# Performance work log

Measured on AMD Instinct MI355X. Metric: run time of the kernel, lower is better.

The kernel has to match this reference:

```python
import jax, jax.numpy as jnp
import numpy as np

N = 100000      # nodes
E = 1600000     # edges
NW = 512        # num_words (input feature dim)
H = 128         # hidden_size
L = 3           # num_layers
G = 256         # num graphs
NEG = 0.2       # GAT leaky_relu slope
EPS = 1e-5      # batchnorm eps


def setup_inputs() -> dict:
    key = jax.random.key(0)
    ks = jax.random.split(key, 20)
    x = jax.random.normal(ks[0], (N, NW), jnp.float32)
    edge_index = jax.random.randint(ks[1], (2, E), 0, N, dtype=jnp.int64)
    edge_attr = jax.random.randint(ks[2], (E,), 0, 8, dtype=jnp.int64)
    batch = jnp.sort(jax.random.randint(ks[3], (N,), 0, G, dtype=jnp.int64))
    edge_emb = jax.random.normal(ks[4], (8, H), jnp.float32) * 0.05
    W0 = jax.random.normal(ks[5], (NW, H), jnp.float32) / np.sqrt(NW)
    W_rest = jax.random.normal(ks[6], (L - 1, H, H), jnp.float32) / np.sqrt(H)
    att_src = jax.random.normal(ks[7], (L, H), jnp.float32) / np.sqrt(H)
    att_dst = jax.random.normal(ks[8], (L, H), jnp.float32) / np.sqrt(H)
    bias = jax.random.normal(ks[9], (L, H), jnp.float32) * 0.02
    gamma = 1.0 + jax.random.normal(ks[10], (L, H), jnp.float32) * 0.1
    beta = jax.random.normal(ks[11], (L, H), jnp.float32) * 0.02
    gate_w1 = jax.random.normal(ks[12], (H, H), jnp.float32) / np.sqrt(H)
    gate_b1 = jnp.zeros((H,), jnp.float32)
    gate_w2 = jax.random.normal(ks[13], (H, 1), jnp.float32) / np.sqrt(H)
    gate_b2 = jnp.zeros((1,), jnp.float32)
    cls_w = jax.random.normal(ks[14], (H, 2), jnp.float32) / np.sqrt(H)
    cls_b = jnp.zeros((2,), jnp.float32)
    return {"x": x, "edge_index": edge_index, "edge_attr": edge_attr, "batch": batch,
            "edge_emb": edge_emb, "W0": W0, "W_rest": W_rest, "att_src": att_src,
            "att_dst": att_dst, "bias": bias, "gamma": gamma, "beta": beta,
            "gate_w1": gate_w1, "gate_b1": gate_b1, "gate_w2": gate_w2,
            "gate_b2": gate_b2, "cls_w": cls_w, "cls_b": cls_b}


def _gat_layer(x, W, a_s, a_d, b, src, dst):
    # PyG GATConv, heads=1, concat=True: h = xW; e_ij = leaky(a_s.h_src + a_d.h_dst)
    h = x @ W                                   # [N, H]
    a_src = h @ a_s                             # [N]
    a_dst = h @ a_d                             # [N]
    e = jax.nn.leaky_relu(a_src[src] + a_dst[dst], NEG)      # [E+N]
    m = jax.ops.segment_max(e, dst, num_segments=N)          # scatter-softmax over dst
    ex = jnp.exp(e - m[dst])
    den = jax.ops.segment_sum(ex, dst, num_segments=N)
    coef = ex / den[dst]                                      # [E+N]
    out = jax.ops.segment_sum(h[src] * coef[:, None], dst, num_segments=N)
    return out + b


def _batchnorm_relu(x, g, bt):
    mu = jnp.mean(x, axis=0)
    var = jnp.mean((x - mu) ** 2, axis=0)      # biased variance (torch BN forward)
    return jax.nn.relu((x - mu) * jax.lax.rsqrt(var + EPS) * g + bt)


def reference(x, edge_index, edge_attr, batch, edge_emb, W0, W_rest, att_src,
              att_dst, bias, gamma, beta, gate_w1, gate_b1, gate_w2, gate_b2,
              cls_w, cls_b):
    _ = edge_emb[edge_attr]  # computed in original module but never used (DCE'd)
    # add self-loops as GATConv does by default
    loop = jnp.arange(N, dtype=edge_index.dtype)
    src = jnp.concatenate([edge_index[0], loop])
    dst = jnp.concatenate([edge_index[1], loop])
    Ws = [W0] + [W_rest[i] for i in range(L - 1)]
    for i in range(L):
        x = _gat_layer(x, Ws[i], att_src[i], att_dst[i], bias[i], src, dst)
        x = _batchnorm_relu(x, gamma[i], beta[i])  # dropout is identity in eval
    # GlobalAttention pooling: gate = MLP(x) -> segment softmax over graphs
    gate = jax.nn.relu(x @ gate_w1 + gate_b1) @ gate_w2 + gate_b2   # [N, 1]
    gate = gate[:, 0]
    gm = jax.ops.segment_max(gate, batch, num_segments=G)
    gex = jnp.exp(gate - gm[batch])
    gden = jax.ops.segment_sum(gex, batch, num_segments=G)
    gden = jnp.where(gden == 0, 1.0, gden)
    coef = gex / gden[batch]
    pooled = jax.ops.segment_sum(x * coef[:, None], batch, num_segments=G)  # [G, H]
    logits = pooled @ cls_w + cls_b
    return jax.nn.log_softmax(logits, axis=-1)
```

## Files before the change

### kernel.cpp

```cpp
#include <hip/hip_runtime.h>

#define kN  100000
#define kE  1600000
#define kNW 512
#define kH  128
#define kL  3
#define kG  256
#define kNEG 0.2f
#define kEPS 1e-5f

static __device__ __forceinline__ float lrelu(float v) { return v >= 0.f ? v : kNEG * v; }

__global__ void count_deg(const int* __restrict__ ei, int* __restrict__ deg, int E) {
    int e = blockIdx.x * 256 + threadIdx.x;
    if (e < E) atomicAdd(&deg[ei[E + e]], 1);
}

__global__ void scan1(const int* __restrict__ deg, int* __restrict__ bsums, int n) {
    __shared__ int sdata[256];
    int b = blockIdx.x, t = threadIdx.x;
    int base = b * 1024 + t * 4;
    int s = 0;
#pragma unroll
    for (int j = 0; j < 4; j++) { int i = base + j; s += (i < n) ? deg[i] : 0; }
    sdata[t] = s; __syncthreads();
    for (int st = 128; st > 0; st >>= 1) { if (t < st) sdata[t] += sdata[t + st]; __syncthreads(); }
    if (t == 0) bsums[b] = sdata[0];
}

__global__ void scan2(int* __restrict__ bsums, int nb, int* __restrict__ row_ptr_last) {
    __shared__ int lds[128];
    int t = threadIdx.x;
    int v = (t < nb) ? bsums[t] : 0;
    lds[t] = v; __syncthreads();
    for (int st = 1; st < 128; st <<= 1) {
        int x = 0;
        if (t >= st) x = lds[t - st];
        __syncthreads();
        if (t >= st) lds[t] += x;
        __syncthreads();
    }
    if (t < nb) bsums[t] = lds[t] - v;
    if (t == nb - 1) row_ptr_last[0] = lds[t];
}

__global__ void scan3(const int* __restrict__ deg, const int* __restrict__ bsums,
                      int* __restrict__ row_ptr, int* __restrict__ cursor, int n) {
    __shared__ int lds[256];
    int b = blockIdx.x, t = threadIdx.x;
    int base = b * 1024 + t * 4;
    int v[4]; int s = 0;
#pragma unroll
    for (int j = 0; j < 4; j++) { int i = base + j; v[j] = (i < n) ? deg[i] : 0; s += v[j]; }
    lds[t] = s; __syncthreads();
    for (int st = 1; st < 256; st <<= 1) {
        int x = 0;
        if (t >= st) x = lds[t - st];
        __syncthreads();
        if (t >= st) lds[t] += x;
        __syncthreads();
    }
    int excl = (t == 0) ? 0 : lds[t - 1];
    excl += bsums[b];
    int run = excl;
#pragma unroll
    for (int j = 0; j < 4; j++) {
        int i = base + j;
        if (i < n) { row_ptr[i] = run; cursor[i] = run; run += v[j]; }
    }
}

__global__ void fill_csr(const int* __restrict__ ei, int* __restrict__ cursor,
                         int* __restrict__ col_src, int E) {
    int e = blockIdx.x * 256 + threadIdx.x;
    if (e < E) {
        int s = ei[e], d = ei[E + e];
        int p = atomicAdd(&cursor[d], 1);
        col_src[p] = s;
    }
}

__global__ __launch_bounds__(256) void gemm128(const float* __restrict__ A,
                                               const float* __restrict__ B,
                                               float* __restrict__ C, int M, int K,
                                               const float* __restrict__ bias, int do_relu) {
    __shared__ float As[32][132];
    __shared__ float Bs[32][128];
    int tid = threadIdx.x;
    int bm = blockIdx.x * 128;
    int ty = tid >> 4;
    int tx = tid & 15;
    float acc[8][8];
#pragma unroll
    for (int i = 0; i < 8; i++)
#pragma unroll
        for (int j = 0; j < 8; j++) acc[i][j] = 0.f;

    for (int k0 = 0; k0 < K; k0 += 32) {
#pragma unroll
        for (int l = 0; l < 4; l++) {
            int f = tid + l * 256;
            int r = f >> 3;
            int c4 = f & 7;
            int gr = bm + r;
            float4 v = make_float4(0.f, 0.f, 0.f, 0.f);
            if (gr < M) v = *(const float4*)(A + (size_t)gr * K + k0 + c4 * 4);
            As[c4 * 4 + 0][r] = v.x;
            As[c4 * 4 + 1][r] = v.y;
            As[c4 * 4 + 2][r] = v.z;
            As[c4 * 4 + 3][r] = v.w;
        }
#pragma unroll
        for (int l = 0; l < 4; l++) {
            int f = tid + l * 256;
            int r = f >> 5;
            int c4 = f & 31;
            *(float4*)&Bs[r][c4 * 4] = *(const float4*)(B + (size_t)(k0 + r) * 128 + c4 * 4);
        }
        __syncthreads();
#pragma unroll
        for (int kk = 0; kk < 32; kk++) {
            float4 a0 = *(float4*)&As[kk][ty * 8];
            float4 a1 = *(float4*)&As[kk][ty * 8 + 4];
            float4 b0 = *(float4*)&Bs[kk][tx * 4];
            float4 b1 = *(float4*)&Bs[kk][64 + tx * 4];
            float aa[8] = {a0.x, a0.y, a0.z, a0.w, a1.x, a1.y, a1.z, a1.w};
            float bb[8] = {b0.x, b0.y, b0.z, b0.w, b1.x, b1.y, b1.z, b1.w};
#pragma unroll
            for (int i = 0; i < 8; i++)
#pragma unroll
                for (int j = 0; j < 8; j++) acc[i][j] += aa[i] * bb[j];
        }
        __syncthreads();
    }
#pragma unroll
    for (int i = 0; i < 8; i++) {
        int gr = bm + ty * 8 + i;
        if (gr >= M) continue;
#pragma unroll
        for (int half = 0; half < 2; half++) {
            int gc = half * 64 + tx * 4;
            float4 v;
            v.x = acc[i][half * 4 + 0]; v.y = acc[i][half * 4 + 1];
            v.z = acc[i][half * 4 + 2]; v.w = acc[i][half * 4 + 3];
            if (bias) { v.x += bias[gc]; v.y += bias[gc + 1]; v.z += bias[gc + 2]; v.w += bias[gc + 3]; }
            if (do_relu) {
                v.x = fmaxf(v.x, 0.f); v.y = fmaxf(v.y, 0.f);
                v.z = fmaxf(v.z, 0.f); v.w = fmaxf(v.w, 0.f);
            }
            *(float4*)(C + (size_t)gr * 128 + gc) = v;
        }
    }
}

__global__ void att_dots(const float* __restrict__ h, const float* __restrict__ ws_,
                         const float* __restrict__ wd_, float* __restrict__ a_s,
                         float* __restrict__ a_d, int n) {
    int v = blockIdx.x * 4 + (threadIdx.x >> 6);
    int lane = threadIdx.x & 63;
    if (v >= n) return;
    float2 hx = ((const float2*)(h + (size_t)v * 128))[lane];
    float2 ws = ((const float2*)ws_)[lane];
    float2 wd = ((const float2*)wd_)[lane];
    float ps = hx.x * ws.x + hx.y * ws.y;
    float pd = hx.x * wd.x + hx.y * wd.y;
#pragma unroll
    for (int off = 32; off; off >>= 1) {
        ps += __shfl_xor(ps, off);
        pd += __shfl_xor(pd, off);
    }
    if (lane == 0) { a_s[v] = ps; a_d[v] = pd; }
}

__global__ void edge_softmax(const int* __restrict__ row_ptr, const int* __restrict__ col_src,
                             const float* __restrict__ a_s, const float* __restrict__ a_d,
                             float* __restrict__ coef, float* __restrict__ coef_self, int n) {
    int v = blockIdx.x * 4 + (threadIdx.x >> 6);
    int lane = threadIdx.x & 63;
    if (v >= n) return;
    int s0 = row_ptr[v], s1 = row_ptr[v + 1];
    float adv = a_d[v];
    float es = lrelu(a_s[v] + adv);
    float mx = es;
    for (int k = s0 + lane; k < s1; k += 64) {
        float e = lrelu(a_s[col_src[k]] + adv);
        coef[k] = e;
        mx = fmaxf(mx, e);
    }
#pragma unroll
    for (int off = 32; off; off >>= 1) mx = fmaxf(mx, __shfl_xor(mx, off));
    float sum = 0.f;
    for (int k = s0 + lane; k < s1; k += 64) {
        float ex = expf(coef[k] - mx);
        coef[k] = ex;
        sum += ex;
    }
    if (lane == 0) sum += expf(es - mx);
#pragma unroll
    for (int off = 32; off; off >>= 1) sum += __shfl_xor(sum, off);
    float inv = 1.f / sum;
    for (int k = s0 + lane; k < s1; k += 64) coef[k] *= inv;
    if (lane == 0) coef_self[v] = expf(es - mx) * inv;
}

__global__ void aggregate(const int* __restrict__ row_ptr, const int* __restrict__ col_src,
                          const float* __restrict__ coef, const float* __restrict__ coef_self,
                          const float* __restrict__ h, const float* __restrict__ bias,
                          float* __restrict__ out, int n) {
    int v = blockIdx.x * 4 + (threadIdx.x >> 6);
    int lane = threadIdx.x & 63;
    if (v >= n) return;
    int s0 = row_ptr[v], s1 = row_ptr[v + 1];
    const float2* h2 = (const float2*)h;
    float cs = coef_self[v];
    float2 hv = h2[(size_t)v * 64 + lane];
    float ax = cs * hv.x, ay = cs * hv.y;
    for (int k = s0; k < s1; k++) {
        int s = col_src[k];
        float c = coef[k];
        float2 hs = h2[(size_t)s * 64 + lane];
        ax += c * hs.x;
        ay += c * hs.y;
    }
    float2 b = ((const float2*)bias)[lane];
    float2 o; o.x = ax + b.x; o.y = ay + b.y;
    ((float2*)out)[(size_t)v * 64 + lane] = o;
}

__global__ void bn_stats(const float* __restrict__ x, double* __restrict__ sums, int n) {
    int col = threadIdx.x & 127;
    int half = threadIdx.x >> 7;
    double s = 0.0, q = 0.0;
    for (int r = blockIdx.x * 2 + half; r < n; r += gridDim.x * 2) {
        float v = x[(size_t)r * 128 + col];
        s += v;
        q += (double)v * (double)v;
    }
    __shared__ double ls[256], lq[256];
    ls[threadIdx.x] = s; lq[threadIdx.x] = q;
    __syncthreads();
    if (half == 0) {
        s += ls[threadIdx.x + 128];
        q += lq[threadIdx.x + 128];
        atomicAdd(&sums[col], s);
        atomicAdd(&sums[128 + col], q);
    }
}

__global__ void bn_finalize(const double* __restrict__ sums, const float* __restrict__ gamma,
                            const float* __restrict__ beta, float* __restrict__ coefs, int n) {
    int c = threadIdx.x;
    if (c < 128) {
        double mu = sums[c] / n;
        double var = sums[128 + c] / n - mu * mu;
        double rs = 1.0 / sqrt(var + (double)kEPS);
        float sc = (float)rs * gamma[c];
        coefs[c] = sc;
        coefs[128 + c] = beta[c] - (float)(mu * rs) * gamma[c];
    }
}

__global__ void bn_apply(float* __restrict__ x, const float* __restrict__ coefs, int n) {
    int idx = blockIdx.x * 256 + threadIdx.x;
    if (idx >= n * 32) return;
    float4 v = ((const float4*)x)[idx];
    int c = (idx & 31) * 4;
    v.x = fmaxf(v.x * coefs[c + 0] + coefs[128 + c + 0], 0.f);
    v.y = fmaxf(v.y * coefs[c + 1] + coefs[128 + c + 1], 0.f);
    v.z = fmaxf(v.z * coefs[c + 2] + coefs[128 + c + 2], 0.f);
    v.w = fmaxf(v.w * coefs[c + 3] + coefs[128 + c + 3], 0.f);
    ((float4*)x)[idx] = v;
}

__global__ void gate_dot(const float* __restrict__ hidden, const float* __restrict__ gw2,
                         const float* __restrict__ gb2, float* __restrict__ gate, int n) {
    int v = blockIdx.x * 4 + (threadIdx.x >> 6);
    int lane = threadIdx.x & 63;
    if (v >= n) return;
    float2 hx = ((const float2*)(hidden + (size_t)v * 128))[lane];
    float2 w = ((const float2*)gw2)[lane];
    float p = hx.x * w.x + hx.y * w.y;
#pragma unroll
    for (int off = 32; off; off >>= 1) p += __shfl_xor(p, off);
    if (lane == 0) gate[v] = p + gb2[0];
}

__global__ void graph_bounds(const int* __restrict__ batch, int* __restrict__ gstart, int n, int g) {
    int i = blockIdx.x * 256 + threadIdx.x;
    if (i > g) return;
    int lo = 0, hi = n;
    while (lo < hi) {
        int mid = (lo + hi) >> 1;
        if (batch[mid] < i) lo = mid + 1; else hi = mid;
    }
    gstart[i] = lo;
}

__global__ __launch_bounds__(512) void pool(const float* __restrict__ x, const float* __restrict__ gate,
                                            const int* __restrict__ gstart, float* __restrict__ pooled) {
    int g = blockIdx.x;
    int t = threadIdx.x;
    int col = t & 127;
    int q = t >> 7;
    int s0 = gstart[g], s1 = gstart[g + 1];
    __shared__ float red[8];
    __shared__ float acc_lds[512];
    float mx = -INFINITY;
    for (int v = s0 + t; v < s1; v += 512) mx = fmaxf(mx, gate[v]);
#pragma unroll
    for (int off = 32; off; off >>= 1) mx = fmaxf(mx, __shfl_xor(mx, off));
    if ((t & 63) == 0) red[t >> 6] = mx;
    __syncthreads();
    mx = fmaxf(fmaxf(fmaxf(red[0], red[1]), fmaxf(red[2], red[3])),
               fmaxf(fmaxf(red[4], red[5]), fmaxf(red[6], red[7])));
    __syncthreads();
    float sum = 0.f;
    for (int v = s0 + t; v < s1; v += 512) sum += expf(gate[v] - mx);
#pragma unroll
    for (int off = 32; off; off >>= 1) sum += __shfl_xor(sum, off);
    if ((t & 63) == 0) red[t >> 6] = sum;
    __syncthreads();
    sum = red[0] + red[1] + red[2] + red[3] + red[4] + red[5] + red[6] + red[7];
    if (sum == 0.f) sum = 1.f;
    float inv = 1.f / sum;
    float acc = 0.f;
    for (int v = s0 + q; v < s1; v += 4) {
        float c = expf(gate[v] - mx) * inv;
        acc += x[(size_t)v * 128 + col] * c;
    }
    acc_lds[t] = acc;
    __syncthreads();
    if (q == 0)
        pooled[(size_t)g * 128 + col] = acc_lds[col] + acc_lds[128 + col] +
                                        acc_lds[256 + col] + acc_lds[384 + col];
}

__global__ void classify(const float* __restrict__ pooled, const float* __restrict__ cls_w,
                         const float* __restrict__ cls_b, float* __restrict__ out, int g_) {
    int g = blockIdx.x * 4 + (threadIdx.x >> 6);
    int lane = threadIdx.x & 63;
    if (g >= g_) return;
    float2 p = ((const float2*)(pooled + (size_t)g * 128))[lane];
    float4 w = ((const float4*)cls_w)[lane];
    float l0 = p.x * w.x + p.y * w.z;
    float l1 = p.x * w.y + p.y * w.w;
#pragma unroll
    for (int off = 32; off; off >>= 1) {
        l0 += __shfl_xor(l0, off);
        l1 += __shfl_xor(l1, off);
    }
    if (lane == 0) {
        l0 += cls_b[0]; l1 += cls_b[1];
        float m = fmaxf(l0, l1);
        float lse = m + logf(expf(l0 - m) + expf(l1 - m));
        out[g * 2 + 0] = l0 - lse;
        out[g * 2 + 1] = l1 - lse;
    }
}

extern "C" void kernel_launch(void* const* d_in, const int* in_sizes, int n_in,
                              void* d_out, int out_size, void* d_ws, size_t ws_size,
                              hipStream_t stream) {
    const float* x        = (const float*)d_in[0];
    const int*   ei       = (const int*)d_in[1];
    const int*   batch    = (const int*)d_in[3];
    const float* W0       = (const float*)d_in[5];
    const float* W_rest   = (const float*)d_in[6];
    const float* att_src  = (const float*)d_in[7];
    const float* att_dst  = (const float*)d_in[8];
    const float* bias     = (const float*)d_in[9];
    const float* gamma    = (const float*)d_in[10];
    const float* beta     = (const float*)d_in[11];
    const float* gate_w1  = (const float*)d_in[12];
    const float* gate_b1  = (const float*)d_in[13];
    const float* gate_w2  = (const float*)d_in[14];
    const float* gate_b2  = (const float*)d_in[15];
    const float* cls_w    = (const float*)d_in[16];
    const float* cls_b    = (const float*)d_in[17];
    float* out = (float*)d_out;

    char* ws = (char*)d_ws;
    size_t off = 0;
    auto take = [&](size_t bytes) -> void* {
        void* p = ws + off;
        off += (bytes + 255) & ~(size_t)255;
        return p;
    };
    float* h         = (float*)take((size_t)kN * kH * 4);
    float* xa        = (float*)take((size_t)kN * kH * 4);
    float* a_s       = (float*)take((size_t)kN * 4);
    float* a_d       = (float*)take((size_t)kN * 4);
    float* coef_self = (float*)take((size_t)kN * 4);
    int*   deg       = (int*)take((size_t)kN * 4);
    int*   cursor    = (int*)take((size_t)kN * 4);
    int*   row_ptr   = (int*)take((size_t)(kN + 1) * 4);
    int*   col_src   = (int*)take((size_t)kE * 4);
    float* coef_csr  = (float*)take((size_t)kE * 4);
    int*   bsums     = (int*)take(1024 * 4);
    double* bn_sums  = (double*)take(256 * 8);
    float* bn_coefs  = (float*)take(256 * 4);
    float* gate      = (float*)take((size_t)kN * 4);
    int*   gstart    = (int*)take((size_t)(kG + 1) * 4);
    float* pooled    = (float*)take((size_t)kG * kH * 4);
    (void)ws_size; (void)in_sizes; (void)n_in; (void)out_size;

    const int NB = (kN + 1023) / 1024;

    hipMemsetAsync(deg, 0, (size_t)kN * 4, stream);
    count_deg<<<(kE + 255) / 256, 256, 0, stream>>>(ei, deg, kE);
    scan1<<<NB, 256, 0, stream>>>(deg, bsums, kN);
    scan2<<<1, 128, 0, stream>>>(bsums, NB, row_ptr + kN);
    scan3<<<NB, 256, 0, stream>>>(deg, bsums, row_ptr, cursor, kN);
    fill_csr<<<(kE + 255) / 256, 256, 0, stream>>>(ei, cursor, col_src, kE);

    const float* xin = x;
    int K = kNW;
    for (int l = 0; l < kL; l++) {
        const float* W = (l == 0) ? W0 : (W_rest + (size_t)(l - 1) * kH * kH);
        gemm128<<<(kN + 127) / 128, 256, 0, stream>>>(xin, W, h, kN, K, nullptr, 0);
        att_dots<<<(kN + 3) / 4, 256, 0, stream>>>(h, att_src + (size_t)l * kH,
                                                   att_dst + (size_t)l * kH, a_s, a_d, kN);
        edge_softmax<<<(kN + 3) / 4, 256, 0, stream>>>(row_ptr, col_src, a_s, a_d,
                                                       coef_csr, coef_self, kN);
        aggregate<<<(kN + 3) / 4, 256, 0, stream>>>(row_ptr, col_src, coef_csr, coef_self,
                                                    h, bias + (size_t)l * kH, xa, kN);
        hipMemsetAsync(bn_sums, 0, 256 * 8, stream);
        bn_stats<<<1024, 256, 0, stream>>>(xa, bn_sums, kN);
        bn_finalize<<<1, 128, 0, stream>>>(bn_sums, gamma + (size_t)l * kH,
                                           beta + (size_t)l * kH, bn_coefs, kN);
        bn_apply<<<((kN * 32) + 255) / 256, 256, 0, stream>>>(xa, bn_coefs, kN);
        xin = xa;
        K = kH;
    }

    gemm128<<<(kN + 127) / 128, 256, 0, stream>>>(xa, gate_w1, h, kN, kH, gate_b1, 1);
    gate_dot<<<(kN + 3) / 4, 256, 0, stream>>>(h, gate_w2, gate_b2, gate, kN);

    graph_bounds<<<2, 256, 0, stream>>>(batch, gstart, kN, kG);
    pool<<<kG, 512, 0, stream>>>(xa, gate, gstart, pooled);
    classify<<<(kG + 3) / 4, 256, 0, stream>>>(pooled, cls_w, cls_b, out, kG);
}
```

Measured before the change: 1.705 ms.

## Replace FP32 SIMT GEMMs with split-bf16 MFMA GEMMs using prepacked operand tiles

Swaps the FP32 shared-memory GEMM for a matrix-core kernel that emulates FP32 with a three-term bf16 hi/lo split (hi*hi + hi*lo + lo*hi). Activations and weights are prepacked into an MFMA fragment layout, and BN-apply now writes the packed bf16 pair for the next layer's GEMM directly. The first-layer K=512 GEMM is split into two K=256 passes that accumulate into the output. This is meant to cut GEMM compute time, at the cost of extra packing passes and workspace traffic and a small loss of accuracy versus true FP32.

New measurement: 1.613 ms. -5.4%, faster.

```diff
diff --git a/kernel.cpp b/kernel.cpp
--- a/kernel.cpp
+++ b/kernel.cpp
@@ -9,7 +9,18 @@
 #define kNEG 0.2f
 #define kEPS 1e-5f
 
+typedef __attribute__((ext_vector_type(8))) short bf16x8;
+typedef __attribute__((ext_vector_type(4))) float f32x4;
+
 static __device__ __forceinline__ float lrelu(float v) { return v >= 0.f ? v : kNEG * v; }
+
+static __device__ __forceinline__ unsigned short bf16rn(float x) {
+    unsigned u = __float_as_uint(x);
+    return (unsigned short)((u + 0x7FFFu + ((u >> 16) & 1u)) >> 16);
+}
+static __device__ __forceinline__ float bf16tof(unsigned short h) {
+    return __uint_as_float(((unsigned)h) << 16);
+}
 
 __global__ void count_deg(const int* __restrict__ ei, int* __restrict__ deg, int E) {
     int e = blockIdx.x * 256 + threadIdx.x;
@@ -80,75 +91,124 @@
     }
 }
 
-__global__ __launch_bounds__(256) void gemm128(const float* __restrict__ A,
-                                               const float* __restrict__ B,
-                                               float* __restrict__ C, int M, int K,
-                                               const float* __restrict__ bias, int do_relu) {
-    __shared__ float As[32][132];
-    __shared__ float Bs[32][128];
+__global__ void pack_a(const float* __restrict__ A, unsigned short* __restrict__ apk,
+                       int Kpitch, int kbase, int NKT) {
+    int g = blockIdx.x * 256 + threadIdx.x;
+    int lane = g & 63;
+    int t2 = g >> 6;
+    int kt = t2 % NKT;
+    int rt = t2 / NKT;
+    int row = rt * 16 + (lane & 15);
+    int k0 = kbase + kt * 32 + (lane >> 4) * 8;
+    const float* src = A + (size_t)row * Kpitch + k0;
+    float4 v0 = *(const float4*)src;
+    float4 v1 = *(const float4*)(src + 4);
+    float v[8] = {v0.x, v0.y, v0.z, v0.w, v1.x, v1.y, v1.z, v1.w};
+    unsigned short h[8], l[8];
+#pragma unroll
+    for (int j = 0; j < 8; j++) {
+        h[j] = bf16rn(v[j]);
+        l[j] = bf16rn(v[j] - bf16tof(h[j]));
+    }
+    size_t slot = ((size_t)(rt * NKT + kt) * 2) * 512 + lane * 8;
+    int4 vhi = make_int4((unsigned)h[0] | ((unsigned)h[1] << 16), (unsigned)h[2] | ((unsigned)h[3] << 16),
+                         (unsigned)h[4] | ((unsigned)h[5] << 16), (unsigned)h[6] | ((unsigned)h[7] << 16));
+    int4 vlo = make_int4((unsigned)l[0] | ((unsigned)l[1] << 16), (unsigned)l[2] | ((unsigned)l[3] << 16),
+                         (unsigned)l[4] | ((unsigned)l[5] << 16), (unsigned)l[6] | ((unsigned)l[7] << 16));
+    *(int4*)(apk + slot) = vhi;
+    *(int4*)(apk + slot + 512) = vlo;
+}
+
+__global__ void pack_b_all(const float* __restrict__ W0, const float* __restrict__ Wr,
+                           const float* __restrict__ Gw1,
+                           unsigned short* __restrict__ b0a, unsigned short* __restrict__ b0b,
+                           unsigned short* __restrict__ b1, unsigned short* __restrict__ b2,
+                           unsigned short* __restrict__ bg) {
+    int bid = blockIdx.x;
+    const float* src; unsigned short* dst; int kbase; int NKT; int lb;
+    if (bid < 16)      { src = W0;            dst = b0a; kbase = 0;   NKT = 8; lb = bid; }
+    else if (bid < 32) { src = W0;            dst = b0b; kbase = 256; NKT = 8; lb = bid - 16; }
+    else if (bid < 40) { src = Wr;            dst = b1;  kbase = 0;   NKT = 4; lb = bid - 32; }
+    else if (bid < 48) { src = Wr + 128*128;  dst = b2;  kbase = 0;   NKT = 4; lb = bid - 40; }
+    else               { src = Gw1;           dst = bg;  kbase = 0;   NKT = 4; lb = bid - 48; }
+    int g = lb * 256 + threadIdx.x;
+    int lane = g & 63;
+    int t2 = g >> 6;
+    int kt = t2 % NKT;
+    int ct = t2 / NKT;
+    int col = ct * 16 + (lane & 15);
+    int k0 = kbase + kt * 32 + (lane >> 4) * 8;
+    unsigned short h[8], l[8];
+#pragma unroll
+    for (int j = 0; j < 8; j++) {
+        float v = src[(size_t)(k0 + j) * 128 + col];
+        h[j] = bf16rn(v);
+        l[j] = bf16rn(v - bf16tof(h[j]));
+    }
+    size_t slot = ((size_t)(ct * NKT + kt) * 2) * 512 + lane * 8;
+    int4 vhi = make_int4((unsigned)h[0] | ((unsigned)h[1] << 16), (unsigned)h[2] | ((unsigned)h[3] << 16),
+                         (unsigned)h[4] | ((unsigned)h[5] << 16), (unsigned)h[6] | ((unsigned)h[7] << 16));
+    int4 vlo = make_int4((unsigned)l[0] | ((unsigned)l[1] << 16), (unsigned)l[2] | ((unsigned)l[3] << 16),
+                         (unsigned)l[4] | ((unsigned)l[5] << 16), (unsigned)l[6] | ((unsigned)l[7] << 16));
+    *(int4*)(dst + slot) = vhi;
+    *(int4*)(dst + slot + 512) = vlo;
+}
+
+__global__ __launch_bounds__(256) void gemm_mfma(const unsigned short* __restrict__ apk,
+                                                 const unsigned short* __restrict__ bpk,
+                                                 float* __restrict__ C, int M, int NKT,
+                                                 int accum, const float* __restrict__ bias,
+                                                 int do_relu) {
     int tid = threadIdx.x;
-    int bm = blockIdx.x * 128;
-    int ty = tid >> 4;
-    int tx = tid & 15;
-    float acc[8][8];
-#pragma unroll
-    for (int i = 0; i < 8; i++)
-#pragma unroll
-        for (int j = 0; j < 8; j++) acc[i][j] = 0.f;
-
-    for (int k0 = 0; k0 < K; k0 += 32) {
-#pragma unroll
-        for (int l = 0; l < 4; l++) {
-            int f = tid + l * 256;
-            int r = f >> 3;
-            int c4 = f & 7;
-            int gr = bm + r;
-            float4 v = make_float4(0.f, 0.f, 0.f, 0.f);
-            if (gr < M) v = *(const float4*)(A + (size_t)gr * K + k0 + c4 * 4);
-            As[c4 * 4 + 0][r] = v.x;
-            As[c4 * 4 + 1][r] = v.y;
-            As[c4 * 4 + 2][r] = v.z;
-            As[c4 * 4 + 3][r] = v.w;
+    int w = tid >> 6, lane = tid & 63;
+    int rt0 = blockIdx.x * 8 + (w >> 1) * 4;
+    int ct0 = (w & 1) * 4;
+    int laneoff = lane * 8;
+    f32x4 acc[4][4];
+#pragma unroll
+    for (int i = 0; i < 4; i++)
+#pragma unroll
+        for (int j = 0; j < 4; j++) acc[i][j] = (f32x4){0.f, 0.f, 0.f, 0.f};
+
+    for (int kt = 0; kt < NKT; ++kt) {
+        bf16x8 Ah[4], Al[4], Bh[4], Bl[4];
+#pragma unroll
+        for (int f = 0; f < 4; f++) {
+            size_t ao = ((size_t)((rt0 + f) * NKT + kt) * 2) * 512 + laneoff;
+            Ah[f] = *(const bf16x8*)(apk + ao);
+            Al[f] = *(const bf16x8*)(apk + ao + 512);
+            size_t bo = ((size_t)((ct0 + f) * NKT + kt) * 2) * 512 + laneoff;
+            Bh[f] = *(const bf16x8*)(bpk + bo);
+            Bl[f] = *(const bf16x8*)(bpk + bo + 512);
         }
 #pragma unroll
-        for (int l = 0; l < 4; l++) {
-            int f = tid + l * 256;
-            int r = f >> 5;
-            int c4 = f & 31;
-            *(float4*)&Bs[r][c4 * 4] = *(const float4*)(B + (size_t)(k0 + r) * 128 + c4 * 4);
-        }
-        __syncthreads();
-#pragma unroll
-        for (int kk = 0; kk < 32; kk++) {
-            float4 a0 = *(float4*)&As[kk][ty * 8];
-            float4 a1 = *(float4*)&As[kk][ty * 8 + 4];
-            float4 b0 = *(float4*)&Bs[kk][tx * 4];
-            float4 b1 = *(float4*)&Bs[kk][64 + tx * 4];
-            float aa[8] = {a0.x, a0.y, a0.z, a0.w, a1.x, a1.y, a1.z, a1.w};
-            float bb[8] = {b0.x, b0.y, b0.z, b0.w, b1.x, b1.y, b1.z, b1.w};
-#pragma unroll
-            for (int i = 0; i < 8; i++)
-#pragma unroll
-                for (int j = 0; j < 8; j++) acc[i][j] += aa[i] * bb[j];
-        }
-        __syncthreads();
-    }
-#pragma unroll
-    for (int i = 0; i < 8; i++) {
-        int gr = bm + ty * 8 + i;
-        if (gr >= M) continue;
-#pragma unroll
-        for (int half = 0; half < 2; half++) {
-            int gc = half * 64 + tx * 4;
-            float4 v;
-            v.x = acc[i][half * 4 + 0]; v.y = acc[i][half * 4 + 1];
-            v.z = acc[i][half * 4 + 2]; v.w = acc[i][half * 4 + 3];
-            if (bias) { v.x += bias[gc]; v.y += bias[gc + 1]; v.z += bias[gc + 2]; v.w += bias[gc + 3]; }
-            if (do_relu) {
-                v.x = fmaxf(v.x, 0.f); v.y = fmaxf(v.y, 0.f);
-                v.z = fmaxf(v.z, 0.f); v.w = fmaxf(v.w, 0.f);
+        for (int i = 0; i < 4; i++)
+#pragma unroll
+            for (int j = 0; j < 4; j++) {
+                acc[i][j] = __builtin_amdgcn_mfma_f32_16x16x32_bf16(Ah[i], Bh[j], acc[i][j], 0, 0, 0);
+                acc[i][j] = __builtin_amdgcn_mfma_f32_16x16x32_bf16(Ah[i], Bl[j], acc[i][j], 0, 0, 0);
+                acc[i][j] = __builtin_amdgcn_mfma_f32_16x16x32_bf16(Al[i], Bh[j], acc[i][j], 0, 0, 0);
             }
-            *(float4*)(C + (size_t)gr * 128 + gc) = v;
+    }
+    int cbase = ct0 * 16 + (lane & 15);
+    int rgrp = (lane >> 4) * 4;
+#pragma unroll
+    for (int i = 0; i < 4; i++) {
+        int rbase = (rt0 + i) * 16 + rgrp;
+#pragma unroll
+        for (int j = 0; j < 4; j++) {
+            int col = cbase + j * 16;
+#pragma unroll
+            for (int r = 0; r < 4; r++) {
+                int row = rbase + r;
+                if (row < M) {
+                    float v = acc[i][j][r];
+                    if (accum) v += C[(size_t)row * 128 + col];
+                    if (bias) v += bias[col];
+                    if (do_relu) v = fmaxf(v, 0.f);
+                    C[(size_t)row * 128 + col] = v;
+                }
+            }
         }
     }
 }
@@ -260,16 +320,35 @@
     }
 }
 
-__global__ void bn_apply(float* __restrict__ x, const float* __restrict__ coefs, int n) {
+__global__ void bn_apply_pack(const float* __restrict__ xin, const float* __restrict__ coefs,
+                              unsigned short* __restrict__ apk, float* __restrict__ xout, int n) {
     int idx = blockIdx.x * 256 + threadIdx.x;
     if (idx >= n * 32) return;
-    float4 v = ((const float4*)x)[idx];
-    int c = (idx & 31) * 4;
+    float4 v = ((const float4*)xin)[idx];
+    int c4 = idx & 31;
+    int r = idx >> 5;
+    int c = c4 * 4;
     v.x = fmaxf(v.x * coefs[c + 0] + coefs[128 + c + 0], 0.f);
     v.y = fmaxf(v.y * coefs[c + 1] + coefs[128 + c + 1], 0.f);
     v.z = fmaxf(v.z * coefs[c + 2] + coefs[128 + c + 2], 0.f);
     v.w = fmaxf(v.w * coefs[c + 3] + coefs[128 + c + 3], 0.f);
-    ((float4*)x)[idx] = v;
+    if (xout) ((float4*)xout)[idx] = v;
+    int rt = r >> 4;
+    int kt = c >> 5;
+    int lane = (r & 15) + (((c >> 3) & 3) << 4);
+    int half = c4 & 1;
+    size_t slot = ((size_t)(rt * 4 + kt) * 2) * 512 + lane * 8 + half * 4;
+    float vv[4] = {v.x, v.y, v.z, v.w};
+    unsigned short h[4], l[4];
+#pragma unroll
+    for (int j = 0; j < 4; j++) {
+        h[j] = bf16rn(vv[j]);
+        l[j] = bf16rn(vv[j] - bf16tof(h[j]));
+    }
+    int2 vhi = make_int2((unsigned)h[0] | ((unsigned)h[1] << 16), (unsigned)h[2] | ((unsigned)h[3] << 16));
+    int2 vlo = make_int2((unsigned)l[0] | ((unsigned)l[1] << 16), (unsigned)l[2] | ((unsigned)l[3] << 16));
+    *(int2*)(apk + slot) = vhi;
+    *(int2*)(apk + slot + 512) = vlo;
 }
 
 __global__ void gate_dot(const float* __restrict__ hidden, const float* __restrict__ gw2,
@@ -386,8 +465,15 @@
         off += (bytes + 255) & ~(size_t)255;
         return p;
     };
+    const int NRT = 6256;
     float* h         = (float*)take((size_t)kN * kH * 4);
     float* xa        = (float*)take((size_t)kN * kH * 4);
+    unsigned short* apk = (unsigned short*)take((size_t)NRT * 8 * 2 * 512 * 2);
+    unsigned short* bpk0a = (unsigned short*)take(8 * 8 * 2 * 512 * 2);
+    unsigned short* bpk0b = (unsigned short*)take(8 * 8 * 2 * 512 * 2);
+    unsigned short* bpk1  = (unsigned short*)take(8 * 4 * 2 * 512 * 2);
+    unsigned short* bpk2  = (unsigned short*)take(8 * 4 * 2 * 512 * 2);
+    unsigned short* bpkg  = (unsigned short*)take(8 * 4 * 2 * 512 * 2);
     float* a_s       = (float*)take((size_t)kN * 4);
     float* a_d       = (float*)take((size_t)kN * 4);
     float* coef_self = (float*)take((size_t)kN * 4);
@@ -405,6 +491,7 @@
     (void)ws_size; (void)in_sizes; (void)n_in; (void)out_size;
 
     const int NB = (kN + 1023) / 1024;
+    const int GEMM_BLKS = (kN + 127) / 128;
 
     hipMemsetAsync(deg, 0, (size_t)kN * 4, stream);
     count_deg<<<(kE + 255) / 256, 256, 0, stream>>>(ei, deg, kE);
@@ -413,11 +500,18 @@
     scan3<<<NB, 256, 0, stream>>>(deg, bsums, row_ptr, cursor, kN);
     fill_csr<<<(kE + 255) / 256, 256, 0, stream>>>(ei, cursor, col_src, kE);
 
-    const float* xin = x;
-    int K = kNW;
+    pack_b_all<<<56, 256, 0, stream>>>(W0, W_rest, gate_w1, bpk0a, bpk0b, bpk1, bpk2, bpkg);
+
+    pack_a<<<6250 * 8 / 4, 256, 0, stream>>>(x, apk, kNW, 0, 8);
+    gemm_mfma<<<GEMM_BLKS, 256, 0, stream>>>(apk, bpk0a, h, kN, 8, 0, nullptr, 0);
+    pack_a<<<6250 * 8 / 4, 256, 0, stream>>>(x, apk, kNW, 256, 8);
+    gemm_mfma<<<GEMM_BLKS, 256, 0, stream>>>(apk, bpk0b, h, kN, 8, 1, nullptr, 0);
+
     for (int l = 0; l < kL; l++) {
-        const float* W = (l == 0) ? W0 : (W_rest + (size_t)(l - 1) * kH * kH);
-        gemm128<<<(kN + 127) / 128, 256, 0, stream>>>(xin, W, h, kN, K, nullptr, 0);
+        if (l > 0) {
+            const unsigned short* bp = (l == 1) ? bpk1 : bpk2;
+            gemm_mfma<<<GEMM_BLKS, 256, 0, stream>>>(apk, bp, h, kN, 4, 0, nullptr, 0);
+        }
         att_dots<<<(kN + 3) / 4, 256, 0, stream>>>(h, att_src + (size_t)l * kH,
                                                    att_dst + (size_t)l * kH, a_s, a_d, kN);
         edge_softmax<<<(kN + 3) / 4, 256, 0, stream>>>(row_ptr, col_src, a_s, a_d,
@@ -428,12 +522,11 @@
         bn_stats<<<1024, 256, 0, stream>>>(xa, bn_sums, kN);
         bn_finalize<<<1, 128, 0, stream>>>(bn_sums, gamma + (size_t)l * kH,
                                            beta + (size_t)l * kH, bn_coefs, kN);
-        bn_apply<<<((kN * 32) + 255) / 256, 256, 0, stream>>>(xa, bn_coefs, kN);
-        xin = xa;
-        K = kH;
-    }
-
-    gemm128<<<(kN + 127) / 128, 256, 0, stream>>>(xa, gate_w1, h, kN, kH, gate_b1, 1);
+        bn_apply_pack<<<((kN * 32) + 255) / 256, 256, 0, stream>>>(
+            xa, bn_coefs, apk, (l == kL - 1) ? xa : nullptr, kN);
+    }
+
+    gemm_mfma<<<GEMM_BLKS, 256, 0, stream>>>(apk, bpkg, h, kN, 4, 0, gate_b1, 1);
     gate_dot<<<(kN + 3) / 4, 256, 0, stream>>>(h, gate_w2, gate_b2, gate, kN);
 
     graph_bounds<<<2, 256, 0, stream>>>(batch, gstart, kN, kG);
```
